# Kernel tuning notes

Measured on AMD Instinct MI355X. Metric: run time of the kernel, lower is better.

## Reference

```python
import jax, jax.numpy as jnp
import numpy as np
from jax import lax

B, C, T, H = 2, 1024, 1536, 16
D = C // H
SCALE = 1.0 / np.sqrt(D).astype(np.float32)
EPS = 1e-5


def setup_inputs() -> dict:
    key = jax.random.key(0)
    ks = jax.random.split(key, 16)
    x = jax.random.normal(ks[0], (B, C, T), jnp.float32)
    y = jax.random.normal(ks[1], (B, C, T), jnp.float32)
    z = jax.random.normal(ks[2], (B, C, T), jnp.float32)
    # valid-prefix mask (B,1,T): sequence lengths T and 2T//3
    lengths = jnp.array([T, 2 * T // 3])
    mask = (jnp.arange(T)[None, None, :] < lengths[:, None, None])
    # depthwise conv weights (groups=C, bias=False): shape (C,1,3)
    qconv_w = 0.1 * jax.random.normal(ks[3], (C, 1, 3), jnp.float32)
    kconv_w = 0.1 * jax.random.normal(ks[4], (C, 1, 3), jnp.float32)
    vconv_w = 0.1 * jax.random.normal(ks[5], (C, 1, 3), jnp.float32)
    # channel LayerNorm affine params, shape (1,C,1)
    qln_g = jnp.ones((1, C, 1), jnp.float32); qln_b = jnp.zeros((1, C, 1), jnp.float32)
    kln_g = jnp.ones((1, C, 1), jnp.float32); kln_b = jnp.zeros((1, C, 1), jnp.float32)
    vln_g = jnp.ones((1, C, 1), jnp.float32); vln_b = jnp.zeros((1, C, 1), jnp.float32)
    # 1x1 convs (= per-timestep linear): weight (C_out, C_in), bias (C,)
    s = 1.0 / np.sqrt(C)
    wq = s * jax.random.normal(ks[6], (C, C), jnp.float32); bq = jnp.zeros((C,), jnp.float32)
    wk = s * jax.random.normal(ks[7], (C, C), jnp.float32); bk = jnp.zeros((C,), jnp.float32)
    wv = s * jax.random.normal(ks[8], (C, C), jnp.float32); bv = jnp.zeros((C,), jnp.float32)
    wp = s * jax.random.normal(ks[9], (C, C), jnp.float32); bp = jnp.zeros((C,), jnp.float32)
    return {"x": x, "y": y, "z": z, "mask": mask,
            "qconv_w": qconv_w, "kconv_w": kconv_w, "vconv_w": vconv_w,
            "qln_g": qln_g, "qln_b": qln_b, "kln_g": kln_g, "kln_b": kln_b,
            "vln_g": vln_g, "vln_b": vln_b,
            "wq": wq, "bq": bq, "wk": wk, "bk": bk, "wv": wv, "bv": bv,
            "wp": wp, "bp": bp}


def _dwconv(x, w, mf):
    # depthwise conv1d, kernel 3, stride 1, pad 1, then mask (MaskedConv1D)
    out = lax.conv_general_dilated(x, w, window_strides=(1,), padding=[(1, 1)],
                                   dimension_numbers=('NCH', 'OIH', 'NCH'),
                                   feature_group_count=C)
    return out * mf


def _cln(x, g, b):
    # LayerNorm over channel dim (dim=1) of (B,C,T)
    mu = jnp.mean(x, axis=1, keepdims=True)
    r = x - mu
    var = jnp.mean(r * r, axis=1, keepdims=True)
    return r * lax.rsqrt(var + EPS) * g + b


def _pw(x, w, b):
    # 1x1 conv: (B,C,T) -> (B,C,T)
    return jnp.einsum('oc,bct->bot', w, x) + b[None, :, None]


def reference(x, y, z, mask, qconv_w, kconv_w, vconv_w,
              qln_g, qln_b, kln_g, kln_b, vln_g, vln_b,
              wq, bq, wk, bk, wv, bv, wp, bp):
    mf = mask.astype(x.dtype)  # (B,1,T); stride=1 so qx_mask == kv_mask == mask
    q = _pw(_cln(_dwconv(x, qconv_w, mf), qln_g, qln_b), wq, bq)
    k = _pw(_cln(_dwconv(y, kconv_w, mf), kln_g, kln_b), wk, bk)
    v = _pw(_cln(_dwconv(z, vconv_w, mf), vln_g, vln_b), wv, bv)
    # (B,C,T) -> (B,H,T,D)
    qh = q.reshape(B, H, D, T).transpose(0, 1, 3, 2)
    kh = k.reshape(B, H, D, T).transpose(0, 1, 3, 2)
    vh = v.reshape(B, H, D, T).transpose(0, 1, 3, 2)
    att = jnp.einsum('bhqd,bhkd->bhqk', qh * SCALE, kh)
    att = jnp.where(mask[:, :, None, :], att, -jnp.inf)
    att = jax.nn.softmax(att, axis=-1)
    out = jnp.einsum('bhqk,bhkd->bhqd', att, vh * mf[:, :, :, None])
    out = out.transpose(0, 1, 3, 2).reshape(B, C, T)
    out = _pw(out, wp, bp) * mf
    return (out, mask)
```

## Files before the change

### kernel.cpp

```cpp
#include <hip/hip_runtime.h>
#include <hip/hip_bf16.h>

#define NB 2
#define NC 1024
#define NT 1536
#define NH 16
#define ND 64
#define NBT 3072
#define LN_EPS 1e-5f
#define BK 32
#define QS2 0.18033688011112042f

typedef __attribute__((ext_vector_type(8))) __bf16 bf16x8;
typedef __attribute__((ext_vector_type(4))) float f32x4;
typedef __attribute__((ext_vector_type(16))) float f32x16;

__device__ __forceinline__ unsigned short f2bf(float f) {
    unsigned u = __float_as_uint(f);
    u += 0x7fffu + ((u >> 16) & 1u);
    return (unsigned short)(u >> 16);
}
__device__ __forceinline__ float bf2f(unsigned short s) {
    return __uint_as_float(((unsigned)s) << 16);
}
__device__ __forceinline__ unsigned pkbf(float a, float b) {
    union { __bf16 h[2]; unsigned u; } r;
    r.h[0] = (__bf16)a; r.h[1] = (__bf16)b;
    return r.u;
}
__device__ __forceinline__ float exp2fast(float x) {
    return __builtin_amdgcn_exp2f(x);
}
__device__ __forceinline__ f32x4 mfma16(bf16x8 a, bf16x8 b, f32x4 c) {
    return __builtin_amdgcn_mfma_f32_16x16x32_bf16(a, b, c, 0, 0, 0);
}
__device__ __forceinline__ f32x16 mfma32(bf16x8 a, bf16x8 b, f32x16 c) {
    return __builtin_amdgcn_mfma_f32_32x32x16_bf16(a, b, c, 0, 0, 0);
}
__device__ __forceinline__ bf16x8 ldbf8(const unsigned short* p) {
    return *reinterpret_cast<const bf16x8*>(p);
}
__device__ __forceinline__ void gload16(const void* g, void* l) {
    __builtin_amdgcn_global_load_lds(
        (const __attribute__((address_space(1))) void*)g,
        (__attribute__((address_space(3))) void*)l, 16, 0, 0);
}
#define WAITV(n) asm volatile("s_waitcnt vmcnt(" #n ")" ::: "memory")
#define BAR()    do { __builtin_amdgcn_s_barrier(); asm volatile("" ::: "memory"); } while (0)


__global__ __launch_bounds__(256) void wcvt_kernel(
    const float* __restrict__ w0, const float* __restrict__ w1,
    const float* __restrict__ w2, const float* __restrict__ w3,
    unsigned short* __restrict__ o0, unsigned short* __restrict__ o1,
    unsigned short* __restrict__ o2, unsigned short* __restrict__ o3)
{
    const float* src; unsigned short* dst;
    switch (blockIdx.y) {
        case 0: src = w0; dst = o0; break;
        case 1: src = w1; dst = o1; break;
        case 2: src = w2; dst = o2; break;
        default: src = w3; dst = o3; break;
    }
    int i = (blockIdx.x * 256 + threadIdx.x) * 4;
    float4 v = *reinterpret_cast<const float4*>(src + i);
    ushort4 r;
    r.x = f2bf(v.x); r.y = f2bf(v.y); r.z = f2bf(v.z); r.w = f2bf(v.w);
    *reinterpret_cast<ushort4*>(dst + i) = r;
}

__global__ __launch_bounds__(1024) void convln_kernel(
    const float* __restrict__ x, const float* __restrict__ y, const float* __restrict__ z,
    const float* __restrict__ qw, const float* __restrict__ kw, const float* __restrict__ vw,
    const float* __restrict__ qg, const float* __restrict__ qb,
    const float* __restrict__ kgm, const float* __restrict__ kbt,
    const float* __restrict__ vg, const float* __restrict__ vb,
    const int* __restrict__ mask,
    unsigned short* __restrict__ xn, unsigned short* __restrict__ yn,
    unsigned short* __restrict__ zn)
{
    __shared__ unsigned short tile[16 * 1026];
    __shared__ float psum[16][65], psq[16][65];
    __shared__ float smu[16], srs[16];

    int b  = blockIdx.y;
    int t0 = blockIdx.x * 16;
    if (mask[b * NT + t0] == 0) return;

    const float* src; const float* cw; const float* g; const float* be;
    unsigned short* dst;
    if (blockIdx.z == 0)      { src = x; cw = qw; g = qg;  be = qb;  dst = xn; }
    else if (blockIdx.z == 1) { src = y; cw = kw; g = kgm; be = kbt; dst = yn; }
    else                      { src = z; cw = vw; g = vg;  be = vb;  dst = zn; }

    int tid = threadIdx.x;
    int tt = tid & 15, cc = tid >> 4;
    int t = t0 + tt;
    float mval = (mask[b * NT + t] != 0) ? 1.f : 0.f;

    const float* sb = src + (size_t)b * NC * NT;
    float sum = 0.f, ssq = 0.f;
    #pragma unroll 4
    for (int c0 = 0; c0 < NC; c0 += 64) {
        int c = c0 + cc;
        const float* xp = sb + (size_t)c * NT;
        float v0 = xp[t];
        float vm = __shfl_up(v0, 1, 16);
        float vp = __shfl_down(v0, 1, 16);
        if (tt == 0)  vm = (t > 0)      ? xp[t - 1] : 0.f;
        if (tt == 15) vp = (t + 1 < NT) ? xp[t + 1] : 0.f;
        float w0 = cw[c * 3], w1 = cw[c * 3 + 1], w2 = cw[c * 3 + 2];
        float conv = (w0 * vm + w1 * v0 + w2 * vp) * mval;
        tile[tt * 1026 + c] = f2bf(conv);
        sum += conv; ssq += conv * conv;
    }
    psum[tt][cc] = sum; psq[tt][cc] = ssq;
    __syncthreads();

    int wv = tid >> 6, ln = tid & 63;
    float s = psum[wv][ln], q2 = psq[wv][ln];
    #pragma unroll
    for (int off = 32; off; off >>= 1) {
        s  += __shfl_xor(s, off);
        q2 += __shfl_xor(q2, off);
    }
    if (ln == 0) {
        float mu = s * (1.f / 1024.f);
        float var = q2 * (1.f / 1024.f) - mu * mu;
        smu[wv] = mu;
        srs[wv] = rsqrtf(var + LN_EPS);
    }
    __syncthreads();

    int c = tid;
    float gc = g[c], ec = be[c];
    unsigned short* db = dst + (size_t)(b * NT + t0) * NC + c;
    #pragma unroll 4
    for (int r = 0; r < 16; ++r) {
        float val = bf2f(tile[r * 1026 + c]);
        db[(size_t)r * NC] = f2bf((val - smu[r]) * srs[r] * gc + ec);
    }
}

__global__ __launch_bounds__(256) void gemm_qkv_kernel(
    const unsigned short* __restrict__ wqb, const unsigned short* __restrict__ wkb,
    const unsigned short* __restrict__ wvb,
    const unsigned short* __restrict__ xn, const unsigned short* __restrict__ yn,
    const unsigned short* __restrict__ zn,
    const float* __restrict__ bq, const float* __restrict__ bk, const float* __restrict__ bv,
    const int* __restrict__ mask,
    unsigned short* __restrict__ qfr, unsigned short* __restrict__ kfr,
    unsigned short* __restrict__ vfr)
{
    __shared__ __align__(16) unsigned short lX[2][128 * BK];
    __shared__ __align__(16) unsigned short lW[2][128 * BK];

    int nb = blockIdx.x * 128;
    {
        int bm = (nb >= NT);
        if (mask[nb - bm * NT + bm * NT] == 0) return;
    }

    int which = blockIdx.z;
    const unsigned short* W = (which == 0) ? wqb : (which == 1) ? wkb : wvb;
    const unsigned short* X = (which == 0) ? xn : (which == 1) ? yn : zn;
    const float* bias = (which == 0) ? bq : (which == 1) ? bk : bv;

    int tid = threadIdx.x;
    int lane = tid & 63, w = tid >> 6;
    int ob = blockIdx.y * 128;

    int srow = w * 16 + (lane >> 2);
    int chunk = ((lane & 3) ^ ((lane >> 3) & 3)) * 8;
    const unsigned short* gX = X + (size_t)(nb + srow) * NC + chunk;
    const unsigned short* gW = W + (size_t)(ob + srow) * NC + chunk;
    unsigned short* lX0 = &lX[0][0] + w * 16 * BK;
    unsigned short* lW0 = &lW[0][0] + w * 16 * BK;

#define QKV_STAGE(buf, k0) do {                                       \
    gload16(gX + (k0),           lX0 + (buf) * 128 * BK);             \
    gload16(gX + (k0) + 64 * NC, lX0 + (buf) * 128 * BK + 64 * BK);   \
    gload16(gW + (k0),           lW0 + (buf) * 128 * BK);             \
    gload16(gW + (k0) + 64 * NC, lW0 + (buf) * 128 * BK + 64 * BK);   \
} while (0)

    int r0 = lane & 15, kg = lane >> 4;
    int kgs = (kg ^ ((r0 >> 1) & 3)) * 8;
    const unsigned short* fW = &lW[0][0] + ((w & 1)  * 64 + r0) * BK + kgs;
    const unsigned short* fX = &lX[0][0] + ((w >> 1) * 64 + r0) * BK + kgs;

    f32x4 acc[4][4];
    #pragma unroll
    for (int i = 0; i < 4; ++i)
        #pragma unroll
        for (int j = 0; j < 4; ++j) acc[i][j] = (f32x4){0.f, 0.f, 0.f, 0.f};

#define QKV_COMPUTE(buf) do {                                                  \
    bf16x8 a_[4], b_[4];                                                       \
    _Pragma("unroll") for (int i = 0; i < 4; ++i)                              \
        a_[i] = ldbf8(fW + (buf) * 128 * BK + i * 16 * BK);                    \
    _Pragma("unroll") for (int i = 0; i < 4; ++i)                              \
        b_[i] = ldbf8(fX + (buf) * 128 * BK + i * 16 * BK);                    \
    _Pragma("unroll") for (int mf = 0; mf < 4; ++mf)                           \
        _Pragma("unroll") for (int nf = 0; nf < 4; ++nf)                       \
            acc[mf][nf] = mfma16(a_[mf], b_[nf], acc[mf][nf]);                 \
} while (0)

    QKV_STAGE(0, 0);
    #pragma unroll 1
    for (int k0 = 0; k0 < NC - 2 * BK; k0 += 2 * BK) {
        QKV_STAGE(1, k0 + BK);
        WAITV(4); BAR();
        QKV_COMPUTE(0);
        BAR();
        QKV_STAGE(0, k0 + 2 * BK);
        WAITV(4); BAR();
        QKV_COMPUTE(1);
        BAR();
    }
    QKV_STAGE(1, NC - BK);
    WAITV(4); BAR();
    QKV_COMPUTE(0);
    WAITV(0); BAR();
    QKV_COMPUTE(1);

    if (which < 2) {
        unsigned short* OUT = (which == 0) ? qfr : kfr;
        #pragma unroll
        for (int mf = 0; mf < 4; ++mf) {
            int o0 = ob + (w & 1) * 64 + mf * 16 + kg * 4;
            int h = o0 >> 6, c0 = o0 & 63;
            int dd = c0 >> 4, hi2 = (c0 >> 3) & 1, j0 = c0 & 7;
            float4 bz = *reinterpret_cast<const float4*>(bias + o0);
            #pragma unroll
            for (int nf = 0; nf < 4; ++nf) {
                int n = nb + (w >> 1) * 64 + nf * 16 + r0;
                int b_ = (n >= NT), t = n - b_ * NT;
                int t32 = t >> 5, ql = t & 31;
                size_t addr = ((size_t)((b_ * NH + h) * 48 + t32)) * 2048
                            + dd * 512 + (hi2 * 32 + ql) * 8 + j0;
                ushort4 st;
                st.x = f2bf(acc[mf][nf][0] + bz.x);
                st.y = f2bf(acc[mf][nf][1] + bz.y);
                st.z = f2bf(acc[mf][nf][2] + bz.z);
                st.w = f2bf(acc[mf][nf][3] + bz.w);
                *reinterpret_cast<ushort4*>(OUT + addr) = st;
            }
        }
    } else {
        #pragma unroll
        for (int mf = 0; mf < 4; ++mf) {
            int o0 = ob + (w & 1) * 64 + mf * 16 + kg * 4;
            int h = o0 >> 6;
            int dch0 = o0 & 63;
            int d0 = dch0 >> 5;
            #pragma unroll
            for (int nf = 0; nf < 4; ++nf) {
                int n = nb + (w >> 1) * 64 + nf * 16 + r0;
                int b_ = (n >= NT), t = n - b_ * NT;
                int t32 = t >> 5, kloc = t & 31;
                int ks = kloc >> 4, r16 = kloc & 15;
                int hi2 = (r16 >> 2) & 1;
                int j = (r16 & 3) + 4 * (r16 >> 3);
                size_t base = ((size_t)((b_ * NH + h) * 48 + t32)) * 2048
                            + d0 * 1024 + ks * 512 + hi2 * 256 + j;
                #pragma unroll
                for (int r = 0; r < 4; ++r) {
                    int ql = (dch0 + r) & 31;
                    vfr[base + ql * 8] = f2bf(acc[mf][nf][r] + bias[o0 + r]);
                }
            }
        }
    }
#undef QKV_STAGE
#undef QKV_COMPUTE
}

__global__ __launch_bounds__(256) void attn_kernel(
    const unsigned short* __restrict__ qfr, const unsigned short* __restrict__ kfr,
    const unsigned short* __restrict__ vfr, const int* __restrict__ mask,
    unsigned short* __restrict__ oatt)
{
    __shared__ float oL[3][64][33];
    __shared__ float mL[3][64], lL[3][64];

    int bid = blockIdx.x;
    int xcd = bid & 7, slot = bid >> 3;
    int hsel = slot / 48, qt = slot - hsel * 48;
    int bh = (hsel < 2) ? (2 * xcd + hsel) : (16 + 2 * xcd + (hsel - 2));
    int b = bh >> 4, h = bh & 15;
    int q0 = qt * 32;

    int lane = threadIdx.x & 63;
    int w = threadIdx.x >> 6;
    int ql = lane & 31;
    int hi = lane >> 5;

    const int* mrow = mask + b * NT;
    int valid = 0;
    #pragma unroll
    for (int i = 0; i < NT / 64; ++i)
        valid += __popcll(__ballot(mrow[lane + 64 * i] != 0));
    if (q0 >= valid) return;
    int ntiles = (valid + 31) >> 5;

    int per = ntiles >> 2, rem = ntiles & 3;
    int tb = w * per + (w < rem ? w : rem);
    int te = tb + per + (w < rem ? 1 : 0);

    const unsigned short* qtile = qfr + ((size_t)(bh * 48 + qt)) * 2048;
    bf16x8 qf[4];
    #pragma unroll
    for (int dd = 0; dd < 4; ++dd) qf[dd] = ldbf8(qtile + dd * 512 + lane * 8);

    const unsigned short* kbh = kfr + (size_t)bh * 48 * 2048;
    const unsigned short* vbh = vfr + (size_t)bh * 48 * 2048;

    const f32x16 z16 = {0.f,0.f,0.f,0.f, 0.f,0.f,0.f,0.f, 0.f,0.f,0.f,0.f, 0.f,0.f,0.f,0.f};
    f32x16 o0 = z16, o1 = z16;
    float m = -1e30f, l = 0.f;

    bf16x8 kf[4];
    if (tb < te) {
        #pragma unroll
        for (int dd = 0; dd < 4; ++dd)
            kf[dd] = ldbf8(kbh + (size_t)tb * 2048 + dd * 512 + lane * 8);
    }

    for (int t = tb; t < te; ++t) {
        int kb = t * 32;
        f32x16 s = z16;
        #pragma unroll
        for (int dd = 0; dd < 4; ++dd) s = mfma32(kf[dd], qf[dd], s);

        if (t + 1 < te) {
            #pragma unroll
            for (int dd = 0; dd < 4; ++dd)
                kf[dd] = ldbf8(kbh + (size_t)(t + 1) * 2048 + dd * 512 + lane * 8);
        }
        bf16x8 vf[2][2];
        #pragma unroll
        for (int d0 = 0; d0 < 2; ++d0)
            #pragma unroll
            for (int ks = 0; ks < 2; ++ks)
                vf[d0][ks] = ldbf8(vbh + (size_t)t * 2048 + d0 * 1024 + ks * 512 + lane * 8);

        if (kb + 32 > valid) {
            #pragma unroll
            for (int r = 0; r < 16; ++r) {
                int kg = kb + (r & 3) + 8 * (r >> 2) + 4 * hi;
                if (kg >= valid) s[r] = -1e30f;
            }
        }
        float mx = fmaxf(fmaxf(fmaxf(s[0], s[1]), fmaxf(s[2], s[3])),
                         fmaxf(fmaxf(s[4], s[5]), fmaxf(s[6], s[7])));
        float my = fmaxf(fmaxf(fmaxf(s[8], s[9]), fmaxf(s[10], s[11])),
                         fmaxf(fmaxf(s[12], s[13]), fmaxf(s[14], s[15])));
        float pmax = fmaxf(mx, my);
        pmax = fmaxf(pmax, __shfl_xor(pmax, 32));
        float pm = pmax * QS2;

        if (__any(pm > m)) {
            float mn = fmaxf(m, pm);
            float scale = exp2fast(m - mn);
            m = mn;
            l *= scale;
            o0 *= scale; o1 *= scale;
        }

        float negm = -m;
        float p[16];
        #pragma unroll
        for (int i = 0; i < 16; ++i)
            p[i] = exp2fast(__builtin_fmaf(s[i], QS2, negm));
        float r0s = (p[0] + p[1]) + (p[2] + p[3]);
        float r1s = (p[4] + p[5]) + (p[6] + p[7]);
        float r2s = (p[8] + p[9]) + (p[10] + p[11]);
        float r3s = (p[12] + p[13]) + (p[14] + p[15]);
        float rs = (r0s + r1s) + (r2s + r3s);
        rs += __shfl_xor(rs, 32);
        l += rs;

        union { unsigned u[4]; bf16x8 v; } A0, A1;
        A0.u[0] = pkbf(p[0],  p[1]);  A0.u[1] = pkbf(p[2],  p[3]);
        A0.u[2] = pkbf(p[4],  p[5]);  A0.u[3] = pkbf(p[6],  p[7]);
        A1.u[0] = pkbf(p[8],  p[9]);  A1.u[1] = pkbf(p[10], p[11]);
        A1.u[2] = pkbf(p[12], p[13]); A1.u[3] = pkbf(p[14], p[15]);

        o0 = mfma32(vf[0][0], A0.v, o0);
        o0 = mfma32(vf[0][1], A1.v, o0);
        o1 = mfma32(vf[1][0], A0.v, o1);
        o1 = mfma32(vf[1][1], A1.v, o1);
    }

    if (w > 0) {
        int wi = w - 1;
        #pragma unroll
        for (int r = 0; r < 16; ++r) {
            oL[wi][lane][r]      = o0[r];
            oL[wi][lane][16 + r] = o1[r];
        }
        mL[wi][lane] = m;
        lL[wi][lane] = l;
    }
    __syncthreads();
    if (w > 0) return;

    float M = m;
    float mw[3], lw[3];
    #pragma unroll
    for (int j = 0; j < 3; ++j) {
        mw[j] = mL[j][lane];
        lw[j] = lL[j][lane];
        M = fmaxf(M, mw[j]);
    }
    float s0 = exp2fast(m - M);
    float L = l * s0;
    o0 *= s0; o1 *= s0;
    #pragma unroll
    for (int j = 0; j < 3; ++j) {
        float sj = exp2fast(mw[j] - M);
        L += lw[j] * sj;
        #pragma unroll
        for (int r = 0; r < 16; ++r) {
            o0[r] += sj * oL[j][lane][r];
            o1[r] += sj * oL[j][lane][16 + r];
        }
    }

    float inv = (L > 0.f) ? (1.f / L) : 0.f;
    unsigned short* ob = oatt + (size_t)(b * NT + q0 + ql) * NC + h * ND;
    #pragma unroll
    for (int g = 0; g < 4; ++g) {
        ushort4 s0v, s1v;
        s0v.x = f2bf(o0[4 * g + 0] * inv); s0v.y = f2bf(o0[4 * g + 1] * inv);
        s0v.z = f2bf(o0[4 * g + 2] * inv); s0v.w = f2bf(o0[4 * g + 3] * inv);
        s1v.x = f2bf(o1[4 * g + 0] * inv); s1v.y = f2bf(o1[4 * g + 1] * inv);
        s1v.z = f2bf(o1[4 * g + 2] * inv); s1v.w = f2bf(o1[4 * g + 3] * inv);
        *reinterpret_cast<ushort4*>(ob + g * 8 + 4 * hi)      = s0v;
        *reinterpret_cast<ushort4*>(ob + 32 + g * 8 + 4 * hi) = s1v;
    }
}

__global__ __launch_bounds__(256) void gemm_out_kernel(
    const unsigned short* __restrict__ oatt, const unsigned short* __restrict__ wpb,
    const float* __restrict__ bp, const int* __restrict__ mask,
    float* __restrict__ out)
{
    __shared__ __align__(16) unsigned short lA[2][128 * BK];
    __shared__ __align__(16) unsigned short lB[2][64 * BK];

    int tid = threadIdx.x;
    int lane = tid & 63, w = tid >> 6;
    int mb  = blockIdx.x * 128;
    int obb = blockIdx.y * 64;
    int r0 = lane & 15, kg = lane >> 4;

    int b_ = (int)(blockIdx.x >= 12);
    size_t obase = (size_t)b_ * NC * NT;

    if (mask[mb] == 0) {
        f32x4 z = (f32x4){0.f, 0.f, 0.f, 0.f};
        #pragma unroll
        for (int mf = 0; mf < 4; ++mf) {
            int bt0 = mb + (w & 1) * 64 + mf * 16 + kg * 4;
            int t0 = bt0 - b_ * NT;
            #pragma unroll
            for (int nf = 0; nf < 2; ++nf) {
                int o = obb + (w >> 1) * 32 + nf * 16 + r0;
                *reinterpret_cast<f32x4*>(out + obase + (size_t)o * NT + t0) = z;
            }
        }
        return;
    }

    int srow = lane >> 2;
    int chunk = ((lane & 3) ^ ((lane >> 3) & 3)) * 8;
    const unsigned short* gA = oatt + (size_t)(mb + w * 32 + srow) * NC + chunk;
    const unsigned short* gB = wpb + (size_t)(obb + w * 16 + srow) * NC + chunk;
    unsigned short* lAb = &lA[0][0] + w * 32 * BK;
    unsigned short* lBb = &lB[0][0] + w * 16 * BK;

#define OUT_STAGE(buf, k0) do {                                        \
    gload16(gA + (k0),           lAb + (buf) * 128 * BK);              \
    gload16(gA + (k0) + 16 * NC, lAb + (buf) * 128 * BK + 16 * BK);    \
    gload16(gB + (k0),           lBb + (buf) * 64 * BK);               \
} while (0)

    int kgs = (kg ^ ((r0 >> 1) & 3)) * 8;
    const unsigned short* fA = &lA[0][0] + ((w & 1) * 64 + r0) * BK + kgs;
    const unsigned short* fB = &lB[0][0] + ((w >> 1) * 32 + r0) * BK + kgs;

    f32x4 acc[4][2];
    #pragma unroll
    for (int i = 0; i < 4; ++i)
        #pragma unroll
        for (int j = 0; j < 2; ++j) acc[i][j] = (f32x4){0.f, 0.f, 0.f, 0.f};

#define OUT_COMPUTE(buf) do {                                                  \
    bf16x8 a_[4], b_[2];                                                       \
    _Pragma("unroll") for (int i = 0; i < 4; ++i)                              \
        a_[i] = ldbf8(fA + (buf) * 128 * BK + i * 16 * BK);                    \
    _Pragma("unroll") for (int j = 0; j < 2; ++j)                              \
        b_[j] = ldbf8(fB + (buf) * 64 * BK + j * 16 * BK);                     \
    _Pragma("unroll") for (int mf = 0; mf < 4; ++mf)                           \
        _Pragma("unroll") for (int nf = 0; nf < 2; ++nf)                       \
            acc[mf][nf] = mfma16(a_[mf], b_[nf], acc[mf][nf]);                 \
} while (0)

    OUT_STAGE(0, 0);
    #pragma unroll 1
    for (int k0 = 0; k0 < NC - 2 * BK; k0 += 2 * BK) {
        OUT_STAGE(1, k0 + BK);
        WAITV(3); BAR();
        OUT_COMPUTE(0);
        BAR();
        OUT_STAGE(0, k0 + 2 * BK);
        WAITV(3); BAR();
        OUT_COMPUTE(1);
        BAR();
    }
    OUT_STAGE(1, NC - BK);
    WAITV(3); BAR();
    OUT_COMPUTE(0);
    WAITV(0); BAR();
    OUT_COMPUTE(1);

    #pragma unroll
    for (int mf = 0; mf < 4; ++mf) {
        int bt0 = mb + (w & 1) * 64 + mf * 16 + kg * 4;
        int4 mv = *reinterpret_cast<const int4*>(mask + bt0);
        float m0 = mv.x ? 1.f : 0.f;
        float m1 = mv.y ? 1.f : 0.f;
        float m2 = mv.z ? 1.f : 0.f;
        float m3 = mv.w ? 1.f : 0.f;
        int t0 = bt0 - b_ * NT;
        #pragma unroll
        for (int nf = 0; nf < 2; ++nf) {
            int o = obb + (w >> 1) * 32 + nf * 16 + r0;
            float bz = bp[o];
            f32x4 vv;
            vv[0] = (acc[mf][nf][0] + bz) * m0;
            vv[1] = (acc[mf][nf][1] + bz) * m1;
            vv[2] = (acc[mf][nf][2] + bz) * m2;
            vv[3] = (acc[mf][nf][3] + bz) * m3;
            *reinterpret_cast<f32x4*>(out + obase + (size_t)o * NT + t0) = vv;
        }
    }
#undef OUT_STAGE
#undef OUT_COMPUTE
}

__global__ __launch_bounds__(256) void maskout_kernel(const int* __restrict__ mask,
                                                      float* __restrict__ out)
{
    int i = blockIdx.x * 256 + threadIdx.x;
    if (i < NBT) out[(size_t)NB * NC * NT + i] = (mask[i] != 0) ? 1.f : 0.f;
}

extern "C" void kernel_launch(void* const* d_in, const int* in_sizes, int n_in,
                              void* d_out, int out_size, void* d_ws, size_t ws_size,
                              hipStream_t stream)
{
    const float* x    = (const float*)d_in[0];
    const float* y    = (const float*)d_in[1];
    const float* z    = (const float*)d_in[2];
    const int*   mask = (const int*)d_in[3];
    const float* qw   = (const float*)d_in[4];
    const float* kw   = (const float*)d_in[5];
    const float* vw   = (const float*)d_in[6];
    const float* qg   = (const float*)d_in[7];
    const float* qb   = (const float*)d_in[8];
    const float* kgm  = (const float*)d_in[9];
    const float* kbt  = (const float*)d_in[10];
    const float* vg   = (const float*)d_in[11];
    const float* vb   = (const float*)d_in[12];
    const float* wq   = (const float*)d_in[13];
    const float* bq   = (const float*)d_in[14];
    const float* wk   = (const float*)d_in[15];
    const float* bk   = (const float*)d_in[16];
    const float* wv   = (const float*)d_in[17];
    const float* bv   = (const float*)d_in[18];
    const float* wp   = (const float*)d_in[19];
    const float* bp   = (const float*)d_in[20];

    unsigned short* xn  = (unsigned short*)d_ws;
    unsigned short* yn  = xn + (size_t)NBT * NC;
    unsigned short* zn  = yn + (size_t)NBT * NC;
    unsigned short* qfr = zn + (size_t)NBT * NC;
    unsigned short* kfr = qfr + (size_t)NBT * NC;
    unsigned short* vfr = kfr + (size_t)NBT * NC;
    unsigned short* wqb = vfr + (size_t)NBT * NC;
    unsigned short* wkb = wqb + (size_t)NC * NC;
    unsigned short* wvb = wkb + (size_t)NC * NC;
    unsigned short* wpb = wvb + (size_t)NC * NC;
    unsigned short* oatt = xn;

    float* out = (float*)d_out;

    wcvt_kernel<<<dim3(1024, 4), 256, 0, stream>>>(wq, wk, wv, wp, wqb, wkb, wvb, wpb);
    convln_kernel<<<dim3(NT / 16, NB, 3), 1024, 0, stream>>>(
        x, y, z, qw, kw, vw, qg, qb, kgm, kbt, vg, vb, mask, xn, yn, zn);
    gemm_qkv_kernel<<<dim3(NBT / 128, NC / 128, 3), 256, 0, stream>>>(
        wqb, wkb, wvb, xn, yn, zn, bq, bk, bv, mask, qfr, kfr, vfr);
    attn_kernel<<<dim3(48 * 32), 256, 0, stream>>>(qfr, kfr, vfr, mask, oatt);
    gemm_out_kernel<<<dim3(NBT / 128, NC / 64), 256, 0, stream>>>(oatt, wpb, bp, mask, out);
    maskout_kernel<<<dim3(NBT / 256), 256, 0, stream>>>(mask, out);
}
```

Before: 129.1 us.

## Deepen GEMM LDS pipeline to four stages and widen conv-LN time tile

New measurement: 120.0 us. -7.0%, faster.

```diff
diff --git a/kernel.cpp b/kernel.cpp
--- a/kernel.cpp
+++ b/kernel.cpp
@@ -79,12 +79,12 @@
     unsigned short* __restrict__ xn, unsigned short* __restrict__ yn,
     unsigned short* __restrict__ zn)
 {
-    __shared__ unsigned short tile[16 * 1026];
-    __shared__ float psum[16][65], psq[16][65];
-    __shared__ float smu[16], srs[16];
+    __shared__ unsigned short tile[32 * 1026];
+    __shared__ float psum[32][33], psq[32][33];
+    __shared__ float smu[32], srs[32];
 
     int b  = blockIdx.y;
-    int t0 = blockIdx.x * 16;
+    int t0 = blockIdx.x * 32;
     if (mask[b * NT + t0] == 0) return;
 
     const float* src; const float* cw; const float* g; const float* be;
@@ -94,21 +94,21 @@
     else                      { src = z; cw = vw; g = vg;  be = vb;  dst = zn; }
 
     int tid = threadIdx.x;
-    int tt = tid & 15, cc = tid >> 4;
+    int tt = tid & 31, cc = tid >> 5;
     int t = t0 + tt;
     float mval = (mask[b * NT + t] != 0) ? 1.f : 0.f;
 
     const float* sb = src + (size_t)b * NC * NT;
     float sum = 0.f, ssq = 0.f;
     #pragma unroll 4
-    for (int c0 = 0; c0 < NC; c0 += 64) {
+    for (int c0 = 0; c0 < NC; c0 += 32) {
         int c = c0 + cc;
         const float* xp = sb + (size_t)c * NT;
         float v0 = xp[t];
-        float vm = __shfl_up(v0, 1, 16);
-        float vp = __shfl_down(v0, 1, 16);
+        float vm = __shfl_up(v0, 1, 32);
+        float vp = __shfl_down(v0, 1, 32);
         if (tt == 0)  vm = (t > 0)      ? xp[t - 1] : 0.f;
-        if (tt == 15) vp = (t + 1 < NT) ? xp[t + 1] : 0.f;
+        if (tt == 31) vp = (t + 1 < NT) ? xp[t + 1] : 0.f;
         float w0 = cw[c * 3], w1 = cw[c * 3 + 1], w2 = cw[c * 3 + 2];
         float conv = (w0 * vm + w1 * v0 + w2 * vp) * mval;
         tile[tt * 1026 + c] = f2bf(conv);
@@ -118,17 +118,18 @@
     __syncthreads();
 
     int wv = tid >> 6, ln = tid & 63;
-    float s = psum[wv][ln], q2 = psq[wv][ln];
-    #pragma unroll
-    for (int off = 32; off; off >>= 1) {
+    int row = 2 * wv + (ln >> 5), col = ln & 31;
+    float s = psum[row][col], q2 = psq[row][col];
+    #pragma unroll
+    for (int off = 16; off; off >>= 1) {
         s  += __shfl_xor(s, off);
         q2 += __shfl_xor(q2, off);
     }
-    if (ln == 0) {
+    if (col == 0) {
         float mu = s * (1.f / 1024.f);
         float var = q2 * (1.f / 1024.f) - mu * mu;
-        smu[wv] = mu;
-        srs[wv] = rsqrtf(var + LN_EPS);
+        smu[row] = mu;
+        srs[row] = rsqrtf(var + LN_EPS);
     }
     __syncthreads();
 
@@ -136,7 +137,7 @@
     float gc = g[c], ec = be[c];
     unsigned short* db = dst + (size_t)(b * NT + t0) * NC + c;
     #pragma unroll 4
-    for (int r = 0; r < 16; ++r) {
+    for (int r = 0; r < 32; ++r) {
         float val = bf2f(tile[r * 1026 + c]);
         db[(size_t)r * NC] = f2bf((val - smu[r]) * srs[r] * gc + ec);
     }
@@ -152,14 +153,11 @@
     unsigned short* __restrict__ qfr, unsigned short* __restrict__ kfr,
     unsigned short* __restrict__ vfr)
 {
-    __shared__ __align__(16) unsigned short lX[2][128 * BK];
-    __shared__ __align__(16) unsigned short lW[2][128 * BK];
+    __shared__ __align__(16) unsigned short lX[4][128 * BK];
+    __shared__ __align__(16) unsigned short lW[4][128 * BK];
 
     int nb = blockIdx.x * 128;
-    {
-        int bm = (nb >= NT);
-        if (mask[nb - bm * NT + bm * NT] == 0) return;
-    }
+    if (mask[nb] == 0) return;
 
     int which = blockIdx.z;
     const unsigned short* W = (which == 0) ? wqb : (which == 1) ? wkb : wvb;
@@ -207,22 +205,19 @@
 } while (0)
 
     QKV_STAGE(0, 0);
+    QKV_STAGE(1, BK);
     #pragma unroll 1
-    for (int k0 = 0; k0 < NC - 2 * BK; k0 += 2 * BK) {
-        QKV_STAGE(1, k0 + BK);
-        WAITV(4); BAR();
-        QKV_COMPUTE(0);
-        BAR();
-        QKV_STAGE(0, k0 + 2 * BK);
-        WAITV(4); BAR();
-        QKV_COMPUTE(1);
-        BAR();
-    }
-    QKV_STAGE(1, NC - BK);
-    WAITV(4); BAR();
-    QKV_COMPUTE(0);
-    WAITV(0); BAR();
-    QKV_COMPUTE(1);
+    for (int i = 0; i < 7; ++i) {
+        int kb = i * 4 * BK;
+        QKV_STAGE(2, kb + 2 * BK); WAITV(8); BAR(); QKV_COMPUTE(0);
+        QKV_STAGE(3, kb + 3 * BK); WAITV(8); BAR(); QKV_COMPUTE(1);
+        QKV_STAGE(0, kb + 4 * BK); WAITV(8); BAR(); QKV_COMPUTE(2);
+        QKV_STAGE(1, kb + 5 * BK); WAITV(8); BAR(); QKV_COMPUTE(3);
+    }
+    QKV_STAGE(2, 30 * BK); WAITV(8); BAR(); QKV_COMPUTE(0);
+    QKV_STAGE(3, 31 * BK); WAITV(8); BAR(); QKV_COMPUTE(1);
+    WAITV(4); BAR(); QKV_COMPUTE(2);
+    WAITV(0); BAR(); QKV_COMPUTE(3);
 
     if (which < 2) {
         unsigned short* OUT = (which == 0) ? qfr : kfr;
@@ -447,8 +442,8 @@
     const float* __restrict__ bp, const int* __restrict__ mask,
     float* __restrict__ out)
 {
-    __shared__ __align__(16) unsigned short lA[2][128 * BK];
-    __shared__ __align__(16) unsigned short lB[2][64 * BK];
+    __shared__ __align__(16) unsigned short lA[4][128 * BK];
+    __shared__ __align__(16) unsigned short lB[4][64 * BK];
 
     int tid = threadIdx.x;
     int lane = tid & 63, w = tid >> 6;
@@ -509,22 +504,19 @@
 } while (0)
 
     OUT_STAGE(0, 0);
+    OUT_STAGE(1, BK);
     #pragma unroll 1
-    for (int k0 = 0; k0 < NC - 2 * BK; k0 += 2 * BK) {
-        OUT_STAGE(1, k0 + BK);
-        WAITV(3); BAR();
-        OUT_COMPUTE(0);
-        BAR();
-        OUT_STAGE(0, k0 + 2 * BK);
-        WAITV(3); BAR();
-        OUT_COMPUTE(1);
-        BAR();
-    }
-    OUT_STAGE(1, NC - BK);
-    WAITV(3); BAR();
-    OUT_COMPUTE(0);
-    WAITV(0); BAR();
-    OUT_COMPUTE(1);
+    for (int i = 0; i < 7; ++i) {
+        int kb = i * 4 * BK;
+        OUT_STAGE(2, kb + 2 * BK); WAITV(6); BAR(); OUT_COMPUTE(0);
+        OUT_STAGE(3, kb + 3 * BK); WAITV(6); BAR(); OUT_COMPUTE(1);
+        OUT_STAGE(0, kb + 4 * BK); WAITV(6); BAR(); OUT_COMPUTE(2);
+        OUT_STAGE(1, kb + 5 * BK); WAITV(6); BAR(); OUT_COMPUTE(3);
+    }
+    OUT_STAGE(2, 30 * BK); WAITV(6); BAR(); OUT_COMPUTE(0);
+    OUT_STAGE(3, 31 * BK); WAITV(6); BAR(); OUT_COMPUTE(1);
+    WAITV(3); BAR(); OUT_COMPUTE(2);
+    WAITV(0); BAR(); OUT_COMPUTE(3);
 
     #pragma unroll
     for (int mf = 0; mf < 4; ++mf) {
@@ -599,7 +591,7 @@
     float* out = (float*)d_out;
 
     wcvt_kernel<<<dim3(1024, 4), 256, 0, stream>>>(wq, wk, wv, wp, wqb, wkb, wvb, wpb);
-    convln_kernel<<<dim3(NT / 16, NB, 3), 1024, 0, stream>>>(
+    convln_kernel<<<dim3(NT / 32, NB, 3), 1024, 0, stream>>>(
         x, y, z, qw, kw, vw, qg, qb, kgm, kbt, vg, vb, mask, xn, yn, zn);
     gemm_qkv_kernel<<<dim3(NBT / 128, NC / 128, 3), 256, 0, stream>>>(
         wqb, wkb, wvb, xn, yn, zn, bq, bk, bv, mask, qfr, kfr, vfr);
```
